# Optimization experiments

Measured on AMD Instinct MI355X. Metric: run time of the kernel, lower is better.

Reference implementation:

```python
import jax, jax.numpy as jnp
import numpy as np

N_NODES = 50000
N_EDGES = 200000
N_GRAPHS = 256
D_IN = 100
H = 384
STEPS = 4
EPS = 1e-5  # torch BatchNorm1d default eps


def setup_inputs() -> dict:
    key = jax.random.key(0)
    ks = jax.random.split(key, 16)
    def nrm(k, shape, s=0.05):
        return jax.random.normal(k, shape, jnp.float32) * s
    return {
        "x": jax.random.normal(ks[0], (N_NODES, D_IN), jnp.float32),
        "edge_index": jax.random.randint(ks[1], (2, N_EDGES), 0, N_NODES, jnp.int32),
        "batch": jnp.sort(jax.random.randint(ks[2], (N_NODES,), 0, N_GRAPHS, jnp.int32)),
        "w_in": nrm(ks[3], (D_IN, H)), "b_in": jnp.zeros((H,), jnp.float32),
        "bn1_g": jnp.ones((H,), jnp.float32), "bn1_b": jnp.zeros((H,), jnp.float32),
        "ggc_w": nrm(ks[4], (STEPS, H, H)),
        "gru_wih": nrm(ks[5], (3 * H, H)), "gru_whh": nrm(ks[6], (3 * H, H)),
        "gru_bih": jnp.zeros((3 * H,), jnp.float32), "gru_bhh": jnp.zeros((3 * H,), jnp.float32),
        "bn2_g": jnp.ones((H,), jnp.float32), "bn2_b": jnp.zeros((H,), jnp.float32),
        "att_w": nrm(ks[7], (H, 1)), "att_b": jnp.zeros((1,), jnp.float32),
        "fc1_w": nrm(ks[8], (H, H)), "fc1_b": jnp.zeros((H,), jnp.float32),
        "bn3_g": jnp.ones((H,), jnp.float32), "bn3_b": jnp.zeros((H,), jnp.float32),
        "fc2_w": nrm(ks[9], (H, H // 2)), "fc2_b": jnp.zeros((H // 2,), jnp.float32),
        "bn4_g": jnp.ones((H // 2,), jnp.float32), "bn4_b": jnp.zeros((H // 2,), jnp.float32),
        "fc3_w": nrm(ks[10], (H // 2, 2)), "fc3_b": jnp.zeros((2,), jnp.float32),
    }


def _bn(x, g, b):
    # training-mode BatchNorm1d: biased batch stats over dim 0
    m = x.mean(0)
    v = x.var(0)
    return (x - m) * jax.lax.rsqrt(v + EPS) * g + b


def reference(x, edge_index, batch, w_in, b_in, bn1_g, bn1_b, ggc_w,
              gru_wih, gru_whh, gru_bih, gru_bhh, bn2_g, bn2_b,
              att_w, att_b, fc1_w, fc1_b, bn3_g, bn3_b,
              fc2_w, fc2_b, bn4_g, bn4_b, fc3_w, fc3_b):
    h = jax.nn.relu(_bn(x @ w_in + b_in, bn1_g, bn1_b))  # [N, H]
    skip = h
    src, dst = edge_index[0], edge_index[1]
    # GatedGraphConv: per-step linear -> scatter-add over edges -> GRUCell
    for i in range(STEPS):
        m = h @ ggc_w[i]                                   # [N, H]
        agg = jax.ops.segment_sum(m[src], dst, num_segments=N_NODES)
        gi = agg @ gru_wih.T + gru_bih                     # [N, 3H]
        gh = h @ gru_whh.T + gru_bhh
        ir, iz, inn = jnp.split(gi, 3, axis=1)
        hr, hz, hn = jnp.split(gh, 3, axis=1)
        r = jax.nn.sigmoid(ir + hr)
        z = jax.nn.sigmoid(iz + hz)
        n = jnp.tanh(inn + r * hn)
        h = (1.0 - z) * n + z * h
    h = jax.nn.relu(_bn(h, bn2_g, bn2_b) + skip)
    # per-graph attention pooling (segment softmax + weighted segment sum)
    logits = (h @ att_w + att_b)[:, 0]                     # [N]
    seg_max = jax.ops.segment_max(logits, batch, num_segments=N_GRAPHS)
    e = jnp.exp(logits - seg_max[batch])
    denom = jax.ops.segment_sum(e, batch, num_segments=N_GRAPHS)
    w = e / denom[batch]
    pooled = jax.ops.segment_sum(w[:, None] * h, batch, num_segments=N_GRAPHS)  # [G, H]
    y = jax.nn.relu(_bn(pooled @ fc1_w + fc1_b, bn3_g, bn3_b))
    y = jax.nn.relu(_bn(y @ fc2_w + fc2_b, bn4_g, bn4_b))
    return y @ fc3_w + fc3_b                               # [G, 2]
```

## Files before the change

### kernel.cpp

```cpp
#include <hip/hip_runtime.h>
#include <math.h>

#define N_NODESC 50000
#define N_EDGESC 200000
#define N_GRAPHSC 256
#define D_INC 100
#define HD 384
#define STEPSC 4
#define BN_EPS 1e-5f

#define FPSCALE 4194304.0f
#define FPINV   (1.0f / 4194304.0f)

#define STATS_ROWS 512
#define STATS_BLOCKS 98

typedef _Float16 h8v __attribute__((ext_vector_type(8)));
typedef _Float16 h4v __attribute__((ext_vector_type(4)));
typedef float f4v __attribute__((ext_vector_type(4)));

static __device__ __forceinline__ float sigmoidf_(float x) { return 1.0f / (1.0f + expf(-x)); }

static __device__ __forceinline__ f4v mfma3(h8v ah, h8v al, h8v bh, h8v bl, f4v c) {
    c = __builtin_amdgcn_mfma_f32_16x16x32_f16(ah, bh, c, 0, 0, 0);
    c = __builtin_amdgcn_mfma_f32_16x16x32_f16(ah, bl, c, 0, 0, 0);
    c = __builtin_amdgcn_mfma_f32_16x16x32_f16(al, bh, c, 0, 0, 0);
    return c;
}

static __device__ __forceinline__ void gload_lds16(const _Float16* g, _Float16* l) {
    __builtin_amdgcn_global_load_lds(
        (const __attribute__((address_space(1))) unsigned int*)g,
        (__attribute__((address_space(3))) unsigned int*)l, 16, 0, 0);
}

static __device__ __forceinline__ int xcd_swz(int orig, int nwg) {
    const int q = nwg >> 3, r = nwg & 7;
    const int xcd = orig & 7, idx = orig >> 3;
    return (xcd < r ? xcd * (q + 1) : r * (q + 1) + (xcd - r) * q) + idx;
}

__global__ __launch_bounds__(256) void gemm64(const float* __restrict__ A,
                                              const float* __restrict__ B,
                                              const float* __restrict__ bias,
                                              float* __restrict__ C,
                                              int M, int K, int N) {
    __shared__ float As[16][68];
    __shared__ float Bs[16][68];
    const int tid = threadIdx.x;
    const int tx = tid & 15, ty = tid >> 4;
    const int m0 = blockIdx.y << 6, n0 = blockIdx.x << 6;
    const int ar = tid >> 2, ac4 = tid & 3;
    const int br = tid >> 4, bc4 = tid & 15;
    float acc[4][4] = {};
    for (int k0 = 0; k0 < K; k0 += 16) {
        float4 av = make_float4(0.f, 0.f, 0.f, 0.f);
        const int arow = m0 + ar, ak = k0 + (ac4 << 2);
        if (arow < M && ak < K) av = *(const float4*)(A + (size_t)arow * K + ak);
        As[(ac4 << 2) + 0][ar] = av.x;
        As[(ac4 << 2) + 1][ar] = av.y;
        As[(ac4 << 2) + 2][ar] = av.z;
        As[(ac4 << 2) + 3][ar] = av.w;
        float4 bv = make_float4(0.f, 0.f, 0.f, 0.f);
        const int bk = k0 + br;
        if (bk < K) bv = *(const float4*)(B + (size_t)bk * N + n0 + (bc4 << 2));
        *(float4*)&Bs[br][bc4 << 2] = bv;
        __syncthreads();
#pragma unroll
        for (int kk = 0; kk < 16; ++kk) {
            const float4 a = *(const float4*)&As[kk][ty << 2];
            const float4 b = *(const float4*)&Bs[kk][tx << 2];
            const float aarr[4] = {a.x, a.y, a.z, a.w};
            const float barr[4] = {b.x, b.y, b.z, b.w};
#pragma unroll
            for (int i = 0; i < 4; ++i)
#pragma unroll
                for (int j = 0; j < 4; ++j) acc[i][j] = fmaf(aarr[i], barr[j], acc[i][j]);
        }
        __syncthreads();
    }
#pragma unroll
    for (int i = 0; i < 4; ++i) {
        const int row = m0 + (ty << 2) + i;
        if (row >= M) continue;
        const int col0 = n0 + (tx << 2);
        float4 out;
        out.x = acc[i][0]; out.y = acc[i][1]; out.z = acc[i][2]; out.w = acc[i][3];
        if (bias) {
            out.x += bias[col0 + 0]; out.y += bias[col0 + 1];
            out.z += bias[col0 + 2]; out.w += bias[col0 + 3];
        }
        *(float4*)(C + (size_t)row * N + col0) = out;
    }
}


__global__ __launch_bounds__(256) void pack_gru_w(const float* __restrict__ w,
                                                  _Float16* __restrict__ PH,
                                                  _Float16* __restrict__ PL) {
    const int i = blockIdx.x * 256 + threadIdx.x;
    if (i >= 3 * 24 * 12 * 64) return;
    const int l = i & 63;
    const int kc = (i >> 6) % 12;
    const int jt = ((i >> 6) / 12) % 24;
    const int g = (i >> 6) / (12 * 24);
    const int row = g * HD + jt * 16 + (l & 15);
    const int k0 = kc * 32 + ((l >> 4) << 3);
    const float* s = w + (size_t)row * HD + k0;
    h8v hi, lo;
#pragma unroll
    for (int e = 0; e < 8; ++e) {
        const float v = s[e];
        hi[e] = (_Float16)v;
        lo[e] = (_Float16)(v - (float)hi[e]);
    }
    *(h8v*)(PH + (size_t)i * 8) = hi;
    *(h8v*)(PL + (size_t)i * 8) = lo;
}

__global__ __launch_bounds__(256) void pack_ggc_w(const float* __restrict__ w,
                                                  _Float16* __restrict__ PH,
                                                  _Float16* __restrict__ PL) {
    const int i = blockIdx.x * 256 + threadIdx.x;
    if (i >= STEPSC * 24 * 12 * 64) return;
    const int l = i & 63;
    const int kc = (i >> 6) % 12;
    const int jt = ((i >> 6) / 12) % 24;
    const int s = (i >> 6) / (12 * 24);
    const int n = jt * 16 + (l & 15);
    const int k0 = kc * 32 + ((l >> 4) << 3);
    h8v hi, lo;
#pragma unroll
    for (int e = 0; e < 8; ++e) {
        const float v = w[((size_t)s * HD + k0 + e) * HD + n];
        hi[e] = (_Float16)v;
        lo[e] = (_Float16)(v - (float)hi[e]);
    }
    *(h8v*)(PH + (size_t)i * 8) = hi;
    *(h8v*)(PL + (size_t)i * 8) = lo;
}

__global__ void deg_count(const int* __restrict__ dst, int* __restrict__ deg) {
    const int e = blockIdx.x * 256 + threadIdx.x;
    if (e < N_EDGESC) atomicAdd(&deg[dst[e]], 1);
}

__global__ __launch_bounds__(1024) void scan_deg(const int* __restrict__ deg,
                                                 int* __restrict__ offs) {
    __shared__ int sums[1024];
    const int t = threadIdx.x;
    const int CH = (N_NODESC + 1023) / 1024;
    const int base = t * CH;
    int s = 0;
    for (int i = 0; i < CH; ++i) {
        const int idx = base + i;
        if (idx < N_NODESC) s += deg[idx];
    }
    sums[t] = s;
    __syncthreads();
    for (int o = 1; o < 1024; o <<= 1) {
        const int v = (t >= o) ? sums[t - o] : 0;
        __syncthreads();
        sums[t] += v;
        __syncthreads();
    }
    int run = (t > 0) ? sums[t - 1] : 0;
    for (int i = 0; i < CH; ++i) {
        const int idx = base + i;
        if (idx < N_NODESC) {
            offs[idx] = run;
            run += deg[idx];
        }
    }
    if (t == 1023) offs[N_NODESC] = run;
}

__global__ void fill_csr(const int* __restrict__ src, const int* __restrict__ dst,
                         const int* __restrict__ offs, int* __restrict__ cursor,
                         int* __restrict__ esrc) {
    const int e = blockIdx.x * 256 + threadIdx.x;
    if (e >= N_EDGESC) return;
    const int d = dst[e];
    const int pos = atomicAdd(&cursor[d], 1);
    esrc[offs[d] + pos] = src[e];
}

__global__ __launch_bounds__(256) void gather_agg_h(const _Float16* __restrict__ mH,
                                                    const _Float16* __restrict__ mL,
                                                    const int* __restrict__ offs,
                                                    const int* __restrict__ esrc,
                                                    _Float16* __restrict__ aggH,
                                                    _Float16* __restrict__ aggL) {
    const int gid = blockIdx.x * 256 + threadIdx.x;
    const int n = gid / 48;
    const int c = gid % 48;
    if (n >= N_NODESC) return;
    const int beg = offs[n], end = offs[n + 1];
    int acc[8] = {};
    for (int i = beg; i < end; ++i) {
        const int s = esrc[i];
        const size_t so = (size_t)s * HD + (c << 3);
        const h8v vh = *(const h8v*)(mH + so);
        const h8v vl = *(const h8v*)(mL + so);
#pragma unroll
        for (int j = 0; j < 8; ++j)
            acc[j] += __float2int_rn(((float)vh[j] + (float)vl[j]) * FPSCALE);
    }
    h8v a, b;
#pragma unroll
    for (int j = 0; j < 8; ++j) {
        const float v = acc[j] * FPINV;
        a[j] = (_Float16)v;
        b[j] = (_Float16)(v - (float)a[j]);
    }
    *(h8v*)(aggH + (size_t)n * HD + (c << 3)) = a;
    *(h8v*)(aggL + (size_t)n * HD + (c << 3)) = b;
}

__global__ __launch_bounds__(256) void ggc_lds(const _Float16* __restrict__ hH,
                                               const _Float16* __restrict__ hL,
                                               const _Float16* __restrict__ wtH,
                                               const _Float16* __restrict__ wtL,
                                               _Float16* __restrict__ mH,
                                               _Float16* __restrict__ mL) {
    __shared__ _Float16 sH[2][2][64][64];
    const int tid = threadIdx.x;
    const int wid = tid >> 6, lane = tid & 63;
    const int lr = lane & 15, lk = lane >> 4;
    const int wr = wid >> 1, wc = wid & 1;
    const int wgid = xcd_swz(blockIdx.x, gridDim.x);
    const int row0 = (wgid / 6) << 6, j0 = (wgid % 6) << 6;
    const int sp = wid >> 1;
    const int srbase = (wid & 1) << 5;
    const int lrow = lane >> 3, ls = lane & 7;
    const _Float16* splane = sp ? hL : hH;

    f4v acc[2][2];
    const f4v z4 = {0.f, 0.f, 0.f, 0.f};
    acc[0][0] = z4; acc[0][1] = z4; acc[1][0] = z4; acc[1][1] = z4;

#define GGC_STAGE(BUF, K0)                                                     \
    _Pragma("unroll")                                                          \
    for (int t4 = 0; t4 < 4; ++t4) {                                           \
        const int row = srbase + (t4 << 3) + lrow;                             \
        const int gk = (K0) + ((ls ^ (row & 7)) << 3);                         \
        const int grow = min(row0 + row, N_NODESC - 1);                        \
        gload_lds16(splane + (size_t)grow * HD + gk,                           \
                    &sH[BUF][sp][srbase + (t4 << 3)][0]);                      \
    }

    GGC_STAGE(0, 0);
    __syncthreads();
    int cur = 0;
    for (int t = 0; t < HD / 64; ++t) {
        if (t + 1 < HD / 64) GGC_STAGE(cur ^ 1, (t + 1) * 64);
#pragma unroll
        for (int kk = 0; kk < 64; kk += 32) {
            h8v fh[2], fl[2], bh[2], bl[2];
#pragma unroll
            for (int sm = 0; sm < 2; ++sm) {
                const int row = wr * 32 + sm * 16 + lr;
                const int s8 = (((kk >> 3) + lk) ^ (row & 7)) << 3;
                fh[sm] = *(const h8v*)&sH[cur][0][row][s8];
                fl[sm] = *(const h8v*)&sH[cur][1][row][s8];
            }
            const int kc = t * 2 + (kk >> 5);
#pragma unroll
            for (int sn = 0; sn < 2; ++sn) {
                const int jt = (j0 >> 4) + wc * 2 + sn;
                const size_t woff = ((size_t)(jt * 12 + kc) << 9) + (lane << 3);
                bh[sn] = *(const h8v*)(wtH + woff);
                bl[sn] = *(const h8v*)(wtL + woff);
            }
            __builtin_amdgcn_s_setprio(1);
#pragma unroll
            for (int sm = 0; sm < 2; ++sm)
#pragma unroll
                for (int sn = 0; sn < 2; ++sn)
                    acc[sm][sn] = mfma3(fh[sm], fl[sm], bh[sn], bl[sn], acc[sm][sn]);
            __builtin_amdgcn_s_setprio(0);
        }
        __syncthreads();
        cur ^= 1;
    }
#pragma unroll
    for (int sm = 0; sm < 2; ++sm)
#pragma unroll
        for (int sn = 0; sn < 2; ++sn) {
            const int col = j0 + wc * 32 + sn * 16 + lr;
#pragma unroll
            for (int j = 0; j < 4; ++j) {
                const int row = row0 + wr * 32 + sm * 16 + lk * 4 + j;
                if (row < N_NODESC) {
                    const size_t off = (size_t)row * HD + col;
                    const float v = acc[sm][sn][j];
                    const _Float16 hh = (_Float16)v;
                    mH[off] = hh;
                    mL[off] = (_Float16)(v - (float)hh);
                }
            }
        }
#undef GGC_STAGE
}

__global__ __launch_bounds__(256) void gru_lds(const _Float16* __restrict__ aH,
                                               const _Float16* __restrict__ aL,
                                               const _Float16* __restrict__ hH,
                                               const _Float16* __restrict__ hL,
                                               const _Float16* __restrict__ wihH,
                                               const _Float16* __restrict__ wihL,
                                               const _Float16* __restrict__ whhH,
                                               const _Float16* __restrict__ whhL,
                                               const float* __restrict__ bih,
                                               const float* __restrict__ bhh,
                                               _Float16* __restrict__ oH,
                                               _Float16* __restrict__ oL) {
    __shared__ _Float16 sA[2][4][64][64];
    const int tid = threadIdx.x;
    const int wid = tid >> 6, lane = tid & 63;
    const int lr = lane & 15, lk = lane >> 4;
    const int wr = wid >> 1, wc = wid & 1;
    const int wgid = xcd_swz(blockIdx.x, gridDim.x);
    const int row0 = (wgid / 6) << 6, j0 = (wgid % 6) << 6;
    const int lrow = lane >> 3, ls = lane & 7;
    const _Float16* splane = (wid == 0) ? aH : (wid == 1) ? aL : (wid == 2) ? hH : hL;

    f4v acc[4][2][2];
    const f4v z4 = {0.f, 0.f, 0.f, 0.f};
#pragma unroll
    for (int g = 0; g < 4; ++g)
#pragma unroll
        for (int a = 0; a < 2; ++a)
#pragma unroll
            for (int b = 0; b < 2; ++b) acc[g][a][b] = z4;

#define GRU_STAGE(BUF, K0)                                                     \
    _Pragma("unroll")                                                          \
    for (int t8 = 0; t8 < 8; ++t8) {                                           \
        const int row = (t8 << 3) + lrow;                                      \
        const int gk = (K0) + ((ls ^ (row & 7)) << 3);                         \
        const int grow = min(row0 + row, N_NODESC - 1);                        \
        gload_lds16(splane + (size_t)grow * HD + gk,                           \
                    &sA[BUF][wid][t8 << 3][0]);                                \
    }

    GRU_STAGE(0, 0);
    __syncthreads();
    int cur = 0;
    for (int t = 0; t < HD / 64; ++t) {
        if (t + 1 < HD / 64) GRU_STAGE(cur ^ 1, (t + 1) * 64);
#pragma unroll
        for (int kk = 0; kk < 64; kk += 32) {
            h8v fAh[2], fAl[2], fHh[2], fHl[2];
#pragma unroll
            for (int sm = 0; sm < 2; ++sm) {
                const int row = wr * 32 + sm * 16 + lr;
                const int s8 = (((kk >> 3) + lk) ^ (row & 7)) << 3;
                fAh[sm] = *(const h8v*)&sA[cur][0][row][s8];
                fAl[sm] = *(const h8v*)&sA[cur][1][row][s8];
                fHh[sm] = *(const h8v*)&sA[cur][2][row][s8];
                fHl[sm] = *(const h8v*)&sA[cur][3][row][s8];
            }
            const int kc = t * 2 + (kk >> 5);
#pragma unroll
            for (int g = 0; g < 3; ++g) {
                h8v BiH[2], BiL[2], BhH[2], BhL[2];
#pragma unroll
                for (int sn = 0; sn < 2; ++sn) {
                    const int jt = (j0 >> 4) + wc * 2 + sn;
                    const size_t woff = ((size_t)((g * 24 + jt) * 12 + kc) << 9) + (lane << 3);
                    BiH[sn] = *(const h8v*)(wihH + woff);
                    BiL[sn] = *(const h8v*)(wihL + woff);
                    BhH[sn] = *(const h8v*)(whhH + woff);
                    BhL[sn] = *(const h8v*)(whhL + woff);
                }
                __builtin_amdgcn_s_setprio(1);
                if (g < 2) {
#pragma unroll
                    for (int sm = 0; sm < 2; ++sm)
#pragma unroll
                        for (int sn = 0; sn < 2; ++sn) {
                            acc[g][sm][sn] = mfma3(fAh[sm], fAl[sm], BiH[sn], BiL[sn], acc[g][sm][sn]);
                            acc[g][sm][sn] = mfma3(fHh[sm], fHl[sm], BhH[sn], BhL[sn], acc[g][sm][sn]);
                        }
                } else {
#pragma unroll
                    for (int sm = 0; sm < 2; ++sm)
#pragma unroll
                        for (int sn = 0; sn < 2; ++sn) {
                            acc[2][sm][sn] = mfma3(fAh[sm], fAl[sm], BiH[sn], BiL[sn], acc[2][sm][sn]);
                            acc[3][sm][sn] = mfma3(fHh[sm], fHl[sm], BhH[sn], BhL[sn], acc[3][sm][sn]);
                        }
                }
                __builtin_amdgcn_s_setprio(0);
            }
        }
        __syncthreads();
        cur ^= 1;
    }
#pragma unroll
    for (int sm = 0; sm < 2; ++sm)
#pragma unroll
        for (int sn = 0; sn < 2; ++sn) {
            const int col = j0 + wc * 32 + sn * 16 + lr;
            const float brz = bih[col] + bhh[col];
            const float bzz = bih[HD + col] + bhh[HD + col];
            const float bni = bih[2 * HD + col];
            const float bnh = bhh[2 * HD + col];
#pragma unroll
            for (int j = 0; j < 4; ++j) {
                const int row = row0 + wr * 32 + sm * 16 + lk * 4 + j;
                if (row < N_NODESC) {
                    const size_t off = (size_t)row * HD + col;
                    const float hold = (float)hH[off] + (float)hL[off];
                    const float r = sigmoidf_(acc[0][sm][sn][j] + brz);
                    const float z = sigmoidf_(acc[1][sm][sn][j] + bzz);
                    const float n = tanhf((acc[2][sm][sn][j] + bni) + r * (acc[3][sm][sn][j] + bnh));
                    const float res = (1.f - z) * n + z * hold;
                    const _Float16 hh = (_Float16)res;
                    oH[off] = hh;
                    oL[off] = (_Float16)(res - (float)hh);
                }
            }
        }
#undef GRU_STAGE
}

__global__ __launch_bounds__(384) void col_stats_partial(const float* __restrict__ X, int M,
                                                         float* __restrict__ pS,
                                                         float* __restrict__ pQ) {
    const int f = threadIdx.x;
    const int b = blockIdx.x;
    const int r0 = b * STATS_ROWS;
    const int r1 = min(r0 + STATS_ROWS, M);
    float s = 0.f, q = 0.f;
    for (int r = r0; r < r1; ++r) {
        const float v = X[(size_t)r * HD + f];
        s += v;
        q += v * v;
    }
    pS[b * HD + f] = s;
    pQ[b * HD + f] = q;
}

__global__ __launch_bounds__(384) void col_stats_h(const _Float16* __restrict__ hH,
                                                   const _Float16* __restrict__ hL, int M,
                                                   float* __restrict__ pS,
                                                   float* __restrict__ pQ) {
    const int f = threadIdx.x;
    const int b = blockIdx.x;
    const int r0 = b * STATS_ROWS;
    const int r1 = min(r0 + STATS_ROWS, M);
    float s = 0.f, q = 0.f;
    for (int r = r0; r < r1; ++r) {
        const size_t off = (size_t)r * HD + f;
        const float v = (float)hH[off] + (float)hL[off];
        s += v;
        q += v * v;
    }
    pS[b * HD + f] = s;
    pQ[b * HD + f] = q;
}

__global__ void bn_stats_final(const float* __restrict__ pS, const float* __restrict__ pQ,
                               const float* __restrict__ g, const float* __restrict__ b,
                               float* __restrict__ scale, float* __restrict__ shift, float invM) {
    const int f = threadIdx.x;
    float s = 0.f, q = 0.f;
    for (int blk = 0; blk < STATS_BLOCKS; ++blk) {
        s += pS[blk * HD + f];
        q += pQ[blk * HD + f];
    }
    const float mean = s * invM;
    const float var = q * invM - mean * mean;
    const float sc = g[f] * rsqrtf(var + BN_EPS);
    scale[f] = sc;
    shift[f] = b[f] - mean * sc;
}

__global__ __launch_bounds__(256) void bn_relu_split(const float* __restrict__ X,
                                                     const float* __restrict__ scale,
                                                     const float* __restrict__ shift,
                                                     _Float16* __restrict__ hH,
                                                     _Float16* __restrict__ hL) {
    const size_t i4 = (size_t)blockIdx.x * 256 + threadIdx.x;
    const int f = (int)((i4 * 4) % HD);
    const float4 v = ((const float4*)X)[i4];
    float r0 = fmaxf(fmaf(v.x, scale[f + 0], shift[f + 0]), 0.f);
    float r1 = fmaxf(fmaf(v.y, scale[f + 1], shift[f + 1]), 0.f);
    float r2 = fmaxf(fmaf(v.z, scale[f + 2], shift[f + 2]), 0.f);
    float r3 = fmaxf(fmaf(v.w, scale[f + 3], shift[f + 3]), 0.f);
    h4v a, b;
    a[0] = (_Float16)r0; b[0] = (_Float16)(r0 - (float)a[0]);
    a[1] = (_Float16)r1; b[1] = (_Float16)(r1 - (float)a[1]);
    a[2] = (_Float16)r2; b[2] = (_Float16)(r2 - (float)a[2]);
    a[3] = (_Float16)r3; b[3] = (_Float16)(r3 - (float)a[3]);
    *(h4v*)(hH + i4 * 4) = a;
    *(h4v*)(hL + i4 * 4) = b;
}

__global__ __launch_bounds__(256) void bn_relu_apply(const float* X,
                                                     const float* __restrict__ scale,
                                                     const float* __restrict__ shift,
                                                     float* h) {
    const size_t i4 = (size_t)blockIdx.x * 256 + threadIdx.x;
    const int f = (int)((i4 * 4) % HD);
    const float4 v = ((const float4*)X)[i4];
    float4 r;
    r.x = fmaxf(fmaf(v.x, scale[f + 0], shift[f + 0]), 0.f);
    r.y = fmaxf(fmaf(v.y, scale[f + 1], shift[f + 1]), 0.f);
    r.z = fmaxf(fmaf(v.z, scale[f + 2], shift[f + 2]), 0.f);
    r.w = fmaxf(fmaf(v.w, scale[f + 3], shift[f + 3]), 0.f);
    ((float4*)h)[i4] = r;
}

__global__ __launch_bounds__(256) void bn_skip_relu_h(const _Float16* __restrict__ hH,
                                                      const _Float16* __restrict__ hL,
                                                      const float* __restrict__ scale,
                                                      const float* __restrict__ shift,
                                                      const float* __restrict__ skip,
                                                      float* __restrict__ out) {
    const size_t i4 = (size_t)blockIdx.x * 256 + threadIdx.x;
    const int f = (int)((i4 * 4) % HD);
    const h4v a = *(const h4v*)(hH + i4 * 4);
    const h4v b = *(const h4v*)(hL + i4 * 4);
    const float4 s = ((const float4*)skip)[i4];
    float4 r;
    r.x = fmaxf(fmaf((float)a[0] + (float)b[0], scale[f + 0], shift[f + 0]) + s.x, 0.f);
    r.y = fmaxf(fmaf((float)a[1] + (float)b[1], scale[f + 1], shift[f + 1]) + s.y, 0.f);
    r.z = fmaxf(fmaf((float)a[2] + (float)b[2], scale[f + 2], shift[f + 2]) + s.z, 0.f);
    r.w = fmaxf(fmaf((float)a[3] + (float)b[3], scale[f + 3], shift[f + 3]) + s.w, 0.f);
    ((float4*)out)[i4] = r;
}

__global__ __launch_bounds__(64) void att_logits(const float* __restrict__ h2,
                                                 const float* __restrict__ att_w,
                                                 const float* __restrict__ att_b,
                                                 float* __restrict__ logits) {
    const int n = blockIdx.x;
    const int l = threadIdx.x;
    float acc = 0.f;
#pragma unroll
    for (int k = 0; k < HD; k += 64) acc += h2[(size_t)n * HD + k + l] * att_w[k + l];
#pragma unroll
    for (int o = 32; o > 0; o >>= 1) acc += __shfl_down(acc, o);
    if (l == 0) logits[n] = acc + att_b[0];
}

__global__ void count_graphs(const int* __restrict__ batch, int* __restrict__ counts) {
    const int n = blockIdx.x * 256 + threadIdx.x;
    if (n < N_NODESC) atomicAdd(&counts[batch[n]], 1);
}

__global__ void scan_offsets(const int* __restrict__ counts, int* __restrict__ offs) {
    __shared__ int tmp[N_GRAPHSC];
    const int t = threadIdx.x;
    tmp[t] = counts[t];
    __syncthreads();
    for (int o = 1; o < N_GRAPHSC; o <<= 1) {
        int v = (t >= o) ? tmp[t - o] : 0;
        __syncthreads();
        tmp[t] += v;
        __syncthreads();
    }
    offs[t] = tmp[t] - counts[t];
}

__global__ __launch_bounds__(384) void pool_graphs(const float* __restrict__ h2,
                                                   const float* __restrict__ logits,
                                                   const int* __restrict__ offs,
                                                   const int* __restrict__ counts,
                                                   float* __restrict__ pooled) {
    const int g = blockIdx.x;
    const int t = threadIdx.x;
    const int s = offs[g], c = counts[g], e = s + c;
    __shared__ float red[384];
    float mx = -1e30f;
    for (int n = s + t; n < e; n += 384) mx = fmaxf(mx, logits[n]);
    red[t] = mx;
    __syncthreads();
    if (t < 128) red[t] = fmaxf(red[t], fmaxf(red[t + 128], red[t + 256]));
    __syncthreads();
    for (int w = 64; w > 0; w >>= 1) {
        if (t < w) red[t] = fmaxf(red[t], red[t + w]);
        __syncthreads();
    }
    mx = red[0];
    __syncthreads();
    float sm = 0.f;
    for (int n = s + t; n < e; n += 384) sm += expf(logits[n] - mx);
    red[t] = sm;
    __syncthreads();
    if (t < 128) red[t] += red[t + 128] + red[t + 256];
    __syncthreads();
    for (int w = 64; w > 0; w >>= 1) {
        if (t < w) red[t] += red[t + w];
        __syncthreads();
    }
    const float denom = red[0];
    const float inv = (c > 0) ? 1.0f / denom : 0.0f;
    float acc = 0.f;
    for (int n = s; n < e; ++n) acc += expf(logits[n] - mx) * h2[(size_t)n * HD + t];
    pooled[(size_t)g * HD + t] = acc * inv;
}

__global__ void fc_small(const float* __restrict__ X, const float* __restrict__ W,
                         const float* __restrict__ bias, float* __restrict__ Y,
                         int K, int N) {
    const int m = blockIdx.x;
    const int n = threadIdx.x;
    if (n >= N) return;
    float acc = bias[n];
    for (int k = 0; k < K; ++k) acc += X[m * K + k] * W[k * N + n];
    Y[m * N + n] = acc;
}

__global__ void bn_small_relu(float* X, int M, int N,
                              const float* __restrict__ g, const float* __restrict__ b) {
    const int f = threadIdx.x;
    if (f >= N) return;
    float s = 0.f, q = 0.f;
    for (int r = 0; r < M; ++r) {
        const float v = X[r * N + f];
        s += v;
        q += v * v;
    }
    const float mean = s / M;
    const float var = q / M - mean * mean;
    const float sc = g[f] * rsqrtf(var + BN_EPS);
    const float sh = b[f] - mean * sc;
    for (int r = 0; r < M; ++r) X[r * N + f] = fmaxf(X[r * N + f] * sc + sh, 0.f);
}

extern "C" void kernel_launch(void* const* d_in, const int* in_sizes, int n_in,
                              void* d_out, int out_size, void* d_ws, size_t ws_size,
                              hipStream_t stream) {
    const float* x       = (const float*)d_in[0];
    const int*   eidx    = (const int*)d_in[1];
    const int*   batch   = (const int*)d_in[2];
    const float* w_in    = (const float*)d_in[3];
    const float* b_in    = (const float*)d_in[4];
    const float* bn1_g   = (const float*)d_in[5];
    const float* bn1_b   = (const float*)d_in[6];
    const float* ggc_w   = (const float*)d_in[7];
    const float* gru_wih = (const float*)d_in[8];
    const float* gru_whh = (const float*)d_in[9];
    const float* gru_bih = (const float*)d_in[10];
    const float* gru_bhh = (const float*)d_in[11];
    const float* bn2_g   = (const float*)d_in[12];
    const float* bn2_b   = (const float*)d_in[13];
    const float* att_w   = (const float*)d_in[14];
    const float* att_b   = (const float*)d_in[15];
    const float* fc1_w   = (const float*)d_in[16];
    const float* fc1_b   = (const float*)d_in[17];
    const float* bn3_g   = (const float*)d_in[18];
    const float* bn3_b   = (const float*)d_in[19];
    const float* fc2_w   = (const float*)d_in[20];
    const float* fc2_b   = (const float*)d_in[21];
    const float* bn4_g   = (const float*)d_in[22];
    const float* bn4_b   = (const float*)d_in[23];
    const float* fc3_w   = (const float*)d_in[24];
    const float* fc3_b   = (const float*)d_in[25];

    const int* src = eidx;
    const int* dst = eidx + N_EDGESC;

    const size_t NH = (size_t)N_NODESC * HD;
    char* p = (char*)d_ws;
    float* R0 = (float*)p; p += NH * sizeof(float);
    float* R1 = (float*)p; p += NH * sizeof(float);
    float* Mreg = (float*)p; p += NH * sizeof(float);
    _Float16* wihP_H = (_Float16*)p; p += 3 * HD * HD * sizeof(_Float16);
    _Float16* wihP_L = (_Float16*)p; p += 3 * HD * HD * sizeof(_Float16);
    _Float16* whhP_H = (_Float16*)p; p += 3 * HD * HD * sizeof(_Float16);
    _Float16* whhP_L = (_Float16*)p; p += 3 * HD * HD * sizeof(_Float16);
    _Float16* ggcP_H = (_Float16*)p; p += (size_t)STEPSC * HD * HD * sizeof(_Float16);
    _Float16* ggcP_L = (_Float16*)p; p += (size_t)STEPSC * HD * HD * sizeof(_Float16);
    float* logits = (float*)p; p += N_NODESC * sizeof(float);
    float* pS = (float*)p; p += STATS_BLOCKS * HD * sizeof(float);
    float* pQ = (float*)p; p += STATS_BLOCKS * HD * sizeof(float);
    float* scale  = (float*)p; p += HD * sizeof(float);
    float* shift  = (float*)p; p += HD * sizeof(float);
    float* scale1 = (float*)p; p += HD * sizeof(float);
    float* shift1 = (float*)p; p += HD * sizeof(float);
    float* pooled = (float*)p; p += N_GRAPHSC * HD * sizeof(float);
    float* y1 = (float*)p; p += N_GRAPHSC * HD * sizeof(float);
    float* y2 = (float*)p; p += N_GRAPHSC * (HD / 2) * sizeof(float);
    int* counts = (int*)p; p += N_GRAPHSC * sizeof(int);
    int* offs = (int*)p; p += N_GRAPHSC * sizeof(int);
    int* deg    = (int*)p; p += N_NODESC * sizeof(int);
    int* eoffs  = (int*)p; p += (N_NODESC + 1) * sizeof(int);
    int* cursor = (int*)p; p += N_NODESC * sizeof(int);
    int* esrc   = (int*)p; p += N_EDGESC * sizeof(int);

    const int nwg = (HD / 64) * ((N_NODESC + 63) / 64);
    const int ew_blocks = (int)(NH / 4 / 256);

    hipMemsetAsync(deg, 0, N_NODESC * sizeof(int), stream);
    hipMemsetAsync(cursor, 0, N_NODESC * sizeof(int), stream);
    deg_count<<<(N_EDGESC + 255) / 256, 256, 0, stream>>>(dst, deg);
    scan_deg<<<1, 1024, 0, stream>>>(deg, eoffs);
    fill_csr<<<(N_EDGESC + 255) / 256, 256, 0, stream>>>(src, dst, eoffs, cursor, esrc);

    pack_gru_w<<<(3 * 24 * 12 * 64 + 255) / 256, 256, 0, stream>>>(gru_wih, wihP_H, wihP_L);
    pack_gru_w<<<(3 * 24 * 12 * 64 + 255) / 256, 256, 0, stream>>>(gru_whh, whhP_H, whhP_L);
    pack_ggc_w<<<(STEPSC * 24 * 12 * 64 + 255) / 256, 256, 0, stream>>>(ggc_w, ggcP_H, ggcP_L);

    gemm64<<<dim3(HD / 64, (N_NODESC + 63) / 64), 256, 0, stream>>>(x, w_in, b_in, R0,
                                                                    N_NODESC, D_INC, HD);
    col_stats_partial<<<STATS_BLOCKS, 384, 0, stream>>>(R0, N_NODESC, pS, pQ);
    bn_stats_final<<<1, 384, 0, stream>>>(pS, pQ, bn1_g, bn1_b, scale1, shift1, 1.0f / N_NODESC);
    bn_relu_split<<<ew_blocks, 256, 0, stream>>>(R0, scale1, shift1, (_Float16*)R1,
                                                 (_Float16*)R1 + NH);

    float* Hcur = R1;
    float* Oth = R0;
    _Float16* aggH = (_Float16*)Mreg;
    _Float16* aggL = aggH + NH;
    for (int s7 = 0; s7 < STEPSC; ++s7) {
        const _Float16* hcH = (const _Float16*)Hcur;
        const _Float16* hcL = (const _Float16*)Hcur + NH;
        _Float16* mH = (_Float16*)Oth;
        _Float16* mL = mH + NH;
        ggc_lds<<<nwg, 256, 0, stream>>>(hcH, hcL,
                                         ggcP_H + (size_t)s7 * HD * HD,
                                         ggcP_L + (size_t)s7 * HD * HD, mH, mL);
        gather_agg_h<<<(N_NODESC * 48) / 256 + 1, 256, 0, stream>>>(mH, mL, eoffs, esrc,
                                                                    aggH, aggL);
        gru_lds<<<nwg, 256, 0, stream>>>(aggH, aggL, hcH, hcL, wihP_H, wihP_L, whhP_H, whhP_L,
                                         gru_bih, gru_bhh, mH, mL);
        float* t = Hcur; Hcur = Oth; Oth = t;
    }

    const _Float16* hfH = (const _Float16*)Hcur;
    const _Float16* hfL = (const _Float16*)Hcur + NH;
    col_stats_h<<<STATS_BLOCKS, 384, 0, stream>>>(hfH, hfL, N_NODESC, pS, pQ);
    bn_stats_final<<<1, 384, 0, stream>>>(pS, pQ, bn2_g, bn2_b, scale, shift, 1.0f / N_NODESC);
    gemm64<<<dim3(HD / 64, (N_NODESC + 63) / 64), 256, 0, stream>>>(x, w_in, b_in, Oth,
                                                                    N_NODESC, D_INC, HD);
    bn_relu_apply<<<ew_blocks, 256, 0, stream>>>(Oth, scale1, shift1, Oth);
    float* hfinal = Mreg;
    bn_skip_relu_h<<<ew_blocks, 256, 0, stream>>>(hfH, hfL, scale, shift, Oth, hfinal);

    att_logits<<<N_NODESC, 64, 0, stream>>>(hfinal, att_w, att_b, logits);
    hipMemsetAsync(counts, 0, N_GRAPHSC * sizeof(int), stream);
    count_graphs<<<(N_NODESC + 255) / 256, 256, 0, stream>>>(batch, counts);
    scan_offsets<<<1, N_GRAPHSC, 0, stream>>>(counts, offs);
    pool_graphs<<<N_GRAPHSC, 384, 0, stream>>>(hfinal, logits, offs, counts, pooled);

    fc_small<<<N_GRAPHSC, 384, 0, stream>>>(pooled, fc1_w, fc1_b, y1, HD, HD);
    bn_small_relu<<<1, 384, 0, stream>>>(y1, N_GRAPHSC, HD, bn3_g, bn3_b);
    fc_small<<<N_GRAPHSC, 192, 0, stream>>>(y1, fc2_w, fc2_b, y2, HD, HD / 2);
    bn_small_relu<<<1, 192, 0, stream>>>(y2, N_GRAPHSC, HD / 2, bn4_g, bn4_b);
    fc_small<<<N_GRAPHSC, 64, 0, stream>>>(y2, fc3_w, fc3_b, (float*)d_out, HD / 2, 2);
}
```

Measured before the change: 2.989 ms.

## Retile GRU kernel per-wave columns, read old h from LDS, fuse skip BN

The GRU GEMM warp tiling changes from 2x2 waves of 32x32 to four waves each owning a 16-column strip across all 64 rows. Each wave now loads one weight fragment per gate instead of two, and the previous hidden state is read from the LDS tile already staged for the K-slice that matches the block's columns, removing a global reload in the epilogue. Separately, the skip-path BN+ReLU is fused into the final skip-add kernel, dropping one elementwise pass over the N×H buffer. The A-fragment register count doubles, which may raise register pressure and reduce occupancy.

```diff
diff --git a/kernel.cpp b/kernel.cpp
--- a/kernel.cpp
+++ b/kernel.cpp
@@ -319,20 +319,21 @@
     const int tid = threadIdx.x;
     const int wid = tid >> 6, lane = tid & 63;
     const int lr = lane & 15, lk = lane >> 4;
-    const int wr = wid >> 1, wc = wid & 1;
+    const int wc = wid;
     const int wgid = xcd_swz(blockIdx.x, gridDim.x);
     const int row0 = (wgid / 6) << 6, j0 = (wgid % 6) << 6;
+    const int col = j0 + wc * 16 + lr;
+    const int tmatch = j0 >> 6;
     const int lrow = lane >> 3, ls = lane & 7;
     const _Float16* splane = (wid == 0) ? aH : (wid == 1) ? aL : (wid == 2) ? hH : hL;
 
-    f4v acc[4][2][2];
+    f4v acc[4][4];
     const f4v z4 = {0.f, 0.f, 0.f, 0.f};
 #pragma unroll
     for (int g = 0; g < 4; ++g)
 #pragma unroll
-        for (int a = 0; a < 2; ++a)
-#pragma unroll
-            for (int b = 0; b < 2; ++b) acc[g][a][b] = z4;
+        for (int a = 0; a < 4; ++a) acc[g][a] = z4;
+    float hold[4][4];
 
 #define GRU_STAGE(BUF, K0)                                                     \
     _Pragma("unroll")                                                          \
@@ -351,10 +352,10 @@
         if (t + 1 < HD / 64) GRU_STAGE(cur ^ 1, (t + 1) * 64);
 #pragma unroll
         for (int kk = 0; kk < 64; kk += 32) {
-            h8v fAh[2], fAl[2], fHh[2], fHl[2];
-#pragma unroll
-            for (int sm = 0; sm < 2; ++sm) {
-                const int row = wr * 32 + sm * 16 + lr;
+            h8v fAh[4], fAl[4], fHh[4], fHl[4];
+#pragma unroll
+            for (int sm = 0; sm < 4; ++sm) {
+                const int row = sm * 16 + lr;
                 const int s8 = (((kk >> 3) + lk) ^ (row & 7)) << 3;
                 fAh[sm] = *(const h8v*)&sA[cur][0][row][s8];
                 fAl[sm] = *(const h8v*)&sA[cur][1][row][s8];
@@ -362,65 +363,63 @@
                 fHl[sm] = *(const h8v*)&sA[cur][3][row][s8];
             }
             const int kc = t * 2 + (kk >> 5);
+            const int jt = (j0 >> 4) + wc;
 #pragma unroll
             for (int g = 0; g < 3; ++g) {
-                h8v BiH[2], BiL[2], BhH[2], BhL[2];
-#pragma unroll
-                for (int sn = 0; sn < 2; ++sn) {
-                    const int jt = (j0 >> 4) + wc * 2 + sn;
-                    const size_t woff = ((size_t)((g * 24 + jt) * 12 + kc) << 9) + (lane << 3);
-                    BiH[sn] = *(const h8v*)(wihH + woff);
-                    BiL[sn] = *(const h8v*)(wihL + woff);
-                    BhH[sn] = *(const h8v*)(whhH + woff);
-                    BhL[sn] = *(const h8v*)(whhL + woff);
-                }
+                const size_t woff = ((size_t)((g * 24 + jt) * 12 + kc) << 9) + (lane << 3);
+                const h8v BiH = *(const h8v*)(wihH + woff);
+                const h8v BiL = *(const h8v*)(wihL + woff);
+                const h8v BhH = *(const h8v*)(whhH + woff);
+                const h8v BhL = *(const h8v*)(whhL + woff);
                 __builtin_amdgcn_s_setprio(1);
                 if (g < 2) {
 #pragma unroll
-                    for (int sm = 0; sm < 2; ++sm)
-#pragma unroll
-                        for (int sn = 0; sn < 2; ++sn) {
-                            acc[g][sm][sn] = mfma3(fAh[sm], fAl[sm], BiH[sn], BiL[sn], acc[g][sm][sn]);
-                            acc[g][sm][sn] = mfma3(fHh[sm], fHl[sm], BhH[sn], BhL[sn], acc[g][sm][sn]);
-                        }
+                    for (int sm = 0; sm < 4; ++sm) {
+                        acc[g][sm] = mfma3(fAh[sm], fAl[sm], BiH, BiL, acc[g][sm]);
+                        acc[g][sm] = mfma3(fHh[sm], fHl[sm], BhH, BhL, acc[g][sm]);
+                    }
                 } else {
 #pragma unroll
-                    for (int sm = 0; sm < 2; ++sm)
-#pragma unroll
-                        for (int sn = 0; sn < 2; ++sn) {
-                            acc[2][sm][sn] = mfma3(fAh[sm], fAl[sm], BiH[sn], BiL[sn], acc[2][sm][sn]);
-                            acc[3][sm][sn] = mfma3(fHh[sm], fHl[sm], BhH[sn], BhL[sn], acc[3][sm][sn]);
-                        }
+                    for (int sm = 0; sm < 4; ++sm) {
+                        acc[2][sm] = mfma3(fAh[sm], fAl[sm], BiH, BiL, acc[2][sm]);
+                        acc[3][sm] = mfma3(fHh[sm], fHl[sm], BhH, BhL, acc[3][sm]);
+                    }
                 }
                 __builtin_amdgcn_s_setprio(0);
             }
         }
+        if (t == tmatch) {
+            const int lc = wc * 16 + lr;
+#pragma unroll
+            for (int sm = 0; sm < 4; ++sm)
+#pragma unroll
+                for (int j = 0; j < 4; ++j) {
+                    const int row = sm * 16 + lk * 4 + j;
+                    const int sc = (((lc >> 3) ^ (row & 7)) << 3) | (lc & 7);
+                    hold[sm][j] = (float)sA[cur][2][row][sc] + (float)sA[cur][3][row][sc];
+                }
+        }
         __syncthreads();
         cur ^= 1;
     }
-#pragma unroll
-    for (int sm = 0; sm < 2; ++sm)
-#pragma unroll
-        for (int sn = 0; sn < 2; ++sn) {
-            const int col = j0 + wc * 32 + sn * 16 + lr;
-            const float brz = bih[col] + bhh[col];
-            const float bzz = bih[HD + col] + bhh[HD + col];
-            const float bni = bih[2 * HD + col];
-            const float bnh = bhh[2 * HD + col];
-#pragma unroll
-            for (int j = 0; j < 4; ++j) {
-                const int row = row0 + wr * 32 + sm * 16 + lk * 4 + j;
-                if (row < N_NODESC) {
-                    const size_t off = (size_t)row * HD + col;
-                    const float hold = (float)hH[off] + (float)hL[off];
-                    const float r = sigmoidf_(acc[0][sm][sn][j] + brz);
-                    const float z = sigmoidf_(acc[1][sm][sn][j] + bzz);
-                    const float n = tanhf((acc[2][sm][sn][j] + bni) + r * (acc[3][sm][sn][j] + bnh));
-                    const float res = (1.f - z) * n + z * hold;
-                    const _Float16 hh = (_Float16)res;
-                    oH[off] = hh;
-                    oL[off] = (_Float16)(res - (float)hh);
-                }
+    const float brz = bih[col] + bhh[col];
+    const float bzz = bih[HD + col] + bhh[HD + col];
+    const float bni = bih[2 * HD + col];
+    const float bnh = bhh[2 * HD + col];
+#pragma unroll
+    for (int sm = 0; sm < 4; ++sm)
+#pragma unroll
+        for (int j = 0; j < 4; ++j) {
+            const int row = row0 + sm * 16 + lk * 4 + j;
+            if (row < N_NODESC) {
+                const size_t off = (size_t)row * HD + col;
+                const float r = sigmoidf_(acc[0][sm][j] + brz);
+                const float z = sigmoidf_(acc[1][sm][j] + bzz);
+                const float n = tanhf((acc[2][sm][j] + bni) + r * (acc[3][sm][j] + bnh));
+                const float res = (1.f - z) * n + z * hold[sm][j];
+                const _Float16 hh = (_Float16)res;
+                oH[off] = hh;
+                oL[off] = (_Float16)(res - (float)hh);
             }
         }
 #undef GRU_STAGE
@@ -499,37 +498,28 @@
     *(h4v*)(hL + i4 * 4) = b;
 }
 
-__global__ __launch_bounds__(256) void bn_relu_apply(const float* X,
-                                                     const float* __restrict__ scale,
-                                                     const float* __restrict__ shift,
-                                                     float* h) {
-    const size_t i4 = (size_t)blockIdx.x * 256 + threadIdx.x;
-    const int f = (int)((i4 * 4) % HD);
-    const float4 v = ((const float4*)X)[i4];
-    float4 r;
-    r.x = fmaxf(fmaf(v.x, scale[f + 0], shift[f + 0]), 0.f);
-    r.y = fmaxf(fmaf(v.y, scale[f + 1], shift[f + 1]), 0.f);
-    r.z = fmaxf(fmaf(v.z, scale[f + 2], shift[f + 2]), 0.f);
-    r.w = fmaxf(fmaf(v.w, scale[f + 3], shift[f + 3]), 0.f);
-    ((float4*)h)[i4] = r;
-}
-
-__global__ __launch_bounds__(256) void bn_skip_relu_h(const _Float16* __restrict__ hH,
-                                                      const _Float16* __restrict__ hL,
-                                                      const float* __restrict__ scale,
-                                                      const float* __restrict__ shift,
-                                                      const float* __restrict__ skip,
-                                                      float* __restrict__ out) {
+__global__ __launch_bounds__(256) void bn_skip_relu_h2(const _Float16* __restrict__ hH,
+                                                       const _Float16* __restrict__ hL,
+                                                       const float* __restrict__ scale,
+                                                       const float* __restrict__ shift,
+                                                       const float* __restrict__ G,
+                                                       const float* __restrict__ scale1,
+                                                       const float* __restrict__ shift1,
+                                                       float* __restrict__ out) {
     const size_t i4 = (size_t)blockIdx.x * 256 + threadIdx.x;
     const int f = (int)((i4 * 4) % HD);
     const h4v a = *(const h4v*)(hH + i4 * 4);
     const h4v b = *(const h4v*)(hL + i4 * 4);
-    const float4 s = ((const float4*)skip)[i4];
+    const float4 g = ((const float4*)G)[i4];
+    const float s0 = fmaxf(fmaf(g.x, scale1[f + 0], shift1[f + 0]), 0.f);
+    const float s1 = fmaxf(fmaf(g.y, scale1[f + 1], shift1[f + 1]), 0.f);
+    const float s2 = fmaxf(fmaf(g.z, scale1[f + 2], shift1[f + 2]), 0.f);
+    const float s3 = fmaxf(fmaf(g.w, scale1[f + 3], shift1[f + 3]), 0.f);
     float4 r;
-    r.x = fmaxf(fmaf((float)a[0] + (float)b[0], scale[f + 0], shift[f + 0]) + s.x, 0.f);
-    r.y = fmaxf(fmaf((float)a[1] + (float)b[1], scale[f + 1], shift[f + 1]) + s.y, 0.f);
-    r.z = fmaxf(fmaf((float)a[2] + (float)b[2], scale[f + 2], shift[f + 2]) + s.z, 0.f);
-    r.w = fmaxf(fmaf((float)a[3] + (float)b[3], scale[f + 3], shift[f + 3]) + s.w, 0.f);
+    r.x = fmaxf(fmaf((float)a[0] + (float)b[0], scale[f + 0], shift[f + 0]) + s0, 0.f);
+    r.y = fmaxf(fmaf((float)a[1] + (float)b[1], scale[f + 1], shift[f + 1]) + s1, 0.f);
+    r.z = fmaxf(fmaf((float)a[2] + (float)b[2], scale[f + 2], shift[f + 2]) + s2, 0.f);
+    r.w = fmaxf(fmaf((float)a[3] + (float)b[3], scale[f + 3], shift[f + 3]) + s3, 0.f);
     ((float4*)out)[i4] = r;
 }
 
@@ -738,9 +728,9 @@
     bn_stats_final<<<1, 384, 0, stream>>>(pS, pQ, bn2_g, bn2_b, scale, shift, 1.0f / N_NODESC);
     gemm64<<<dim3(HD / 64, (N_NODESC + 63) / 64), 256, 0, stream>>>(x, w_in, b_in, Oth,
                                                                     N_NODESC, D_INC, HD);
-    bn_relu_apply<<<ew_blocks, 256, 0, stream>>>(Oth, scale1, shift1, Oth);
     float* hfinal = Mreg;
-    bn_skip_relu_h<<<ew_blocks, 256, 0, stream>>>(hfH, hfL, scale, shift, Oth, hfinal);
+    bn_skip_relu_h2<<<ew_blocks, 256, 0, stream>>>(hfH, hfL, scale, shift, Oth,
+                                                   scale1, shift1, hfinal);
 
     att_logits<<<N_NODESC, 64, 0, stream>>>(hfinal, att_w, att_b, logits);
     hipMemsetAsync(counts, 0, N_GRAPHSC * sizeof(int), stream);
```

Result: faster. 2.781 ms (-7.0%).
